# Kernel optimization log

Hardware: AMD Instinct MI355X
Metric: run time of the kernel (lower is better)

The kernel has to match this reference:

```python
import jax, jax.numpy as jnp
import numpy as np

NBINS = 256


def _getmask(mi):
    # mi: [h, w] image already scaled to [0, 255]
    # torch.histc(mi, bins=256, min=0, max=255): values outside [0,255] ignored
    hist = jax.lax.stop_gradient(
        jnp.histogram(mi, bins=NBINS, range=(0.0, 255.0))[0].astype(jnp.float32)
    )
    # mask_output[i] = sum_j |j - i| * hist[j]  -> small 256x256 matvec
    j = jnp.arange(NBINS, dtype=jnp.float32)
    dist = jnp.abs(j[:, None] - j[None, :])  # [256, 256]
    mask_output = dist @ hist                 # [256]
    # mask[image==i] = mask_output[i]; only exact-integer pixels in [0,255] match
    r = jnp.round(mi)
    valid = (mi == r) & (r >= 0.0) & (r <= 255.0)
    idx = jnp.clip(r, 0.0, 255.0).astype(jnp.int32)
    mask = jnp.where(valid, mask_output[idx], 0.0)
    # if mask.max()==0: return zeros; else return the (scaled) image itself
    return jnp.where(mask.max() == 0.0, jnp.zeros_like(mi), mi)


def _forward(image_irr, image_vis):
    irr = image_irr * 255.0
    _vis = image_vis * 255.0  # computed but unused in the original forward
    mi = irr[:, 0, :, :]                       # [b, h, w]
    masked = jax.vmap(_getmask)(mi) / 255.0    # [b, h, w]
    msk_ir = masked[:, None, :, :]             # [b, 1, h, w]
    msk = jnp.stack([msk_ir, 1.0 - msk_ir], axis=0)  # [2, b, 1, h, w]
    msks = jax.nn.softmax(msk, axis=0)
    return msks[0], msks[1]


def setup_inputs() -> dict:
    key = jax.random.key(0)
    k1, k2 = jax.random.split(key)
    shape = (16, 1, 1024, 1024)
    # quantized pixels so that image*255 is (mostly) exactly integer,
    # matching the module's implicit assumption (histc + equality tests)
    image_irr = jax.random.randint(k1, shape, 0, 256).astype(jnp.float32) / 255.0
    image_vis = jax.random.randint(k2, shape, 0, 256).astype(jnp.float32) / 255.0
    return {"image_irr": image_irr, "image_vis": image_vis}


def reference(image_irr, image_vis):
    return _forward(image_irr, image_vis)
```

## Files before the change

kernel.cpp:

```cpp
#include <hip/hip_runtime.h>
#include <stdint.h>

#define NBINS 256
#define BATCH 16
#define HW (1024*1024)
#define NPIX (BATCH * HW)
#define SCAN_BLOCKS 64

__global__ __launch_bounds__(256) void scan_kernel(const float* __restrict__ in,
                                                   uint2* __restrict__ partials) {
    __shared__ int smin[256], smax[256];
    __shared__ unsigned sval[256];
    const int tid = threadIdx.x;
    const int batch = blockIdx.y;

    int minb = 0x7FFF, maxb = -1;
    unsigned valid = 0;

    const float4* src = (const float4*)(in + (size_t)batch * HW) + (size_t)blockIdx.x * 4096;
    for (int i = tid; i < 4096; i += 256) {
        float4 x = src[i];
        float v[4] = {x.x, x.y, x.z, x.w};
#pragma unroll
        for (int k = 0; k < 4; ++k) {
            float mi = v[k] * 255.0f;
            if (mi >= 0.0f && mi <= 255.0f) {
                int b = (int)(mi * (256.0f / 255.0f));
                if (b > 255) b = 255;
                minb = min(minb, b);
                maxb = max(maxb, b);
                valid |= (mi == rintf(mi)) ? 1u : 0u;
            }
        }
    }
    smin[tid] = minb; smax[tid] = maxb; sval[tid] = valid;
    __syncthreads();
    for (int s = 128; s > 0; s >>= 1) {
        if (tid < s) {
            smin[tid] = min(smin[tid], smin[tid + s]);
            smax[tid] = max(smax[tid], smax[tid + s]);
            sval[tid] |= sval[tid + s];
        }
        __syncthreads();
    }
    if (tid == 0) {
        uint2 p;
        p.x = ((unsigned)(smin[0] & 0xFFFF) << 16) | (unsigned)(smax[0] & 0xFFFF);
        p.y = sval[0];
        partials[batch * SCAN_BLOCKS + blockIdx.x] = p;
    }
}

__global__ __launch_bounds__(64) void flag_kernel(const uint2* __restrict__ partials,
                                                  unsigned* __restrict__ flags) {
    const int b = blockIdx.x;
    const int t = threadIdx.x;
    uint2 p = partials[b * SCAN_BLOCKS + t];
    int minb = (int)(short)(p.x >> 16);
    int maxb = (int)(short)(p.x & 0xFFFF);
    unsigned valid = p.y;
#pragma unroll
    for (int off = 32; off > 0; off >>= 1) {
        minb = min(minb, __shfl_xor(minb, off));
        maxb = max(maxb, __shfl_xor(maxb, off));
        valid |= (unsigned)__shfl_xor((int)valid, off);
    }
    if (t == 0) flags[b] = (valid && (minb != maxb)) ? 1u : 0u;
}

__device__ __forceinline__ void softmax2(float x, unsigned flag, float& o0, float& o1) {
    float mi = x * 255.0f;
    float m = flag ? (mi / 255.0f) : 0.0f;
    float a = m;
    float b = 1.0f - m;
    float M = fmaxf(a, b);
    float e0 = expf(a - M);
    float e1 = expf(b - M);
    float s = e0 + e1;
    o0 = e0 / s;
    o1 = e1 / s;
}

__global__ __launch_bounds__(256) void out_kernel(const float* __restrict__ in,
                                                  const unsigned* __restrict__ flags,
                                                  float* __restrict__ out) {
    const size_t i4 = (size_t)blockIdx.x * 256 + threadIdx.x;
    const int batch = (int)(i4 >> 18);
    const unsigned f = flags[batch];
    float4 x = ((const float4*)in)[i4];
    float4 o0, o1;
    softmax2(x.x, f, o0.x, o1.x);
    softmax2(x.y, f, o0.y, o1.y);
    softmax2(x.z, f, o0.z, o1.z);
    softmax2(x.w, f, o0.w, o1.w);
    ((float4*)out)[i4] = o0;
    ((float4*)(out + (size_t)NPIX))[i4] = o1;
}

extern "C" void kernel_launch(void* const* d_in, const int* in_sizes, int n_in,
                              void* d_out, int out_size, void* d_ws, size_t ws_size,
                              hipStream_t stream) {
    const float* irr = (const float*)d_in[0];
    float* out = (float*)d_out;

    uint2* partials = (uint2*)d_ws;
    unsigned* flags = (unsigned*)(partials + BATCH * SCAN_BLOCKS);

    scan_kernel<<<dim3(SCAN_BLOCKS, BATCH), 256, 0, stream>>>(irr, partials);
    flag_kernel<<<BATCH, 64, 0, stream>>>(partials, flags);
    out_kernel<<<NPIX / 4 / 256, 256, 0, stream>>>(irr, flags, out);
}
```

Measured before the change: 230.5 us.

## Early-exit scan via global atomics once per-batch mask decision is known

The per-batch scan now accumulates min/max bin and validity into global atomics chunk by chunk. Every block stops reading as soon as the batch is known to have an exact-integer pixel and more than one occupied bin. This removes the separate flag kernel and most of the scan's reads on typical inputs, at the cost of a memset launch and atomic traffic. The output kernel also uses a simplified closed-form two-way softmax and nontemporal loads and stores.

```diff
diff --git a/kernel.cpp b/kernel.cpp
--- a/kernel.cpp
+++ b/kernel.cpp
@@ -1,25 +1,31 @@
 #include <hip/hip_runtime.h>
 #include <stdint.h>
 
-#define NBINS 256
 #define BATCH 16
 #define HW (1024*1024)
 #define NPIX (BATCH * HW)
-#define SCAN_BLOCKS 64
+#define SBLK 64
+
+typedef float vf4 __attribute__((ext_vector_type(4)));
+
+struct BState { unsigned valid, maxp1, maxc, done; };
 
 __global__ __launch_bounds__(256) void scan_kernel(const float* __restrict__ in,
-                                                   uint2* __restrict__ partials) {
-    __shared__ int smin[256], smax[256];
-    __shared__ unsigned sval[256];
+                                                   BState* __restrict__ st) {
     const int tid = threadIdx.x;
     const int batch = blockIdx.y;
+    BState* s = st + batch;
+    const vf4* src = (const vf4*)(in + (size_t)batch * HW) + (size_t)blockIdx.x * 4096;
+    __shared__ int sdone;
 
-    int minb = 0x7FFF, maxb = -1;
-    unsigned valid = 0;
+    for (int c = 0; c < 16; ++c) {
+        if (tid == 0)
+            sdone = (int)__hip_atomic_load(&s->done, __ATOMIC_RELAXED, __HIP_MEMORY_SCOPE_AGENT);
+        __syncthreads();
+        if (sdone) return;
 
-    const float4* src = (const float4*)(in + (size_t)batch * HW) + (size_t)blockIdx.x * 4096;
-    for (int i = tid; i < 4096; i += 256) {
-        float4 x = src[i];
+        vf4 x = src[c * 256 + tid];
+        int minb = 0x7FFF, maxb = -1, valid = 0;
         float v[4] = {x.x, x.y, x.z, x.w};
 #pragma unroll
         for (int k = 0; k < 4; ++k) {
@@ -29,72 +35,57 @@
                 if (b > 255) b = 255;
                 minb = min(minb, b);
                 maxb = max(maxb, b);
-                valid |= (mi == rintf(mi)) ? 1u : 0u;
+                valid |= (mi == rintf(mi)) ? 1 : 0;
             }
         }
-    }
-    smin[tid] = minb; smax[tid] = maxb; sval[tid] = valid;
-    __syncthreads();
-    for (int s = 128; s > 0; s >>= 1) {
-        if (tid < s) {
-            smin[tid] = min(smin[tid], smin[tid + s]);
-            smax[tid] = max(smax[tid], smax[tid + s]);
-            sval[tid] |= sval[tid + s];
+#pragma unroll
+        for (int off = 32; off > 0; off >>= 1) {
+            minb  = min(minb, __shfl_xor(minb, off));
+            maxb  = max(maxb, __shfl_xor(maxb, off));
+            valid |= __shfl_xor(valid, off);
+        }
+        if ((tid & 63) == 0) {
+            if (maxb >= 0) {
+                atomicMax(&s->maxp1, (unsigned)(maxb + 1));
+                atomicMax(&s->maxc,  (unsigned)(256 - minb));
+            }
+            if (valid) atomicOr(&s->valid, 1u);
         }
         __syncthreads();
-    }
-    if (tid == 0) {
-        uint2 p;
-        p.x = ((unsigned)(smin[0] & 0xFFFF) << 16) | (unsigned)(smax[0] & 0xFFFF);
-        p.y = sval[0];
-        partials[batch * SCAN_BLOCKS + blockIdx.x] = p;
+        if (tid == 0) {
+            unsigned v2 = __hip_atomic_load(&s->valid, __ATOMIC_RELAXED, __HIP_MEMORY_SCOPE_AGENT);
+            unsigned mp = __hip_atomic_load(&s->maxp1, __ATOMIC_RELAXED, __HIP_MEMORY_SCOPE_AGENT);
+            unsigned mc = __hip_atomic_load(&s->maxc,  __ATOMIC_RELAXED, __HIP_MEMORY_SCOPE_AGENT);
+            if (v2 && (mp + mc > 257))
+                __hip_atomic_store(&s->done, 1u, __ATOMIC_RELAXED, __HIP_MEMORY_SCOPE_AGENT);
+        }
     }
 }
 
-__global__ __launch_bounds__(64) void flag_kernel(const uint2* __restrict__ partials,
-                                                  unsigned* __restrict__ flags) {
-    const int b = blockIdx.x;
-    const int t = threadIdx.x;
-    uint2 p = partials[b * SCAN_BLOCKS + t];
-    int minb = (int)(short)(p.x >> 16);
-    int maxb = (int)(short)(p.x & 0xFFFF);
-    unsigned valid = p.y;
-#pragma unroll
-    for (int off = 32; off > 0; off >>= 1) {
-        minb = min(minb, __shfl_xor(minb, off));
-        maxb = max(maxb, __shfl_xor(maxb, off));
-        valid |= (unsigned)__shfl_xor((int)valid, off);
-    }
-    if (t == 0) flags[b] = (valid && (minb != maxb)) ? 1u : 0u;
-}
-
-__device__ __forceinline__ void softmax2(float x, unsigned flag, float& o0, float& o1) {
+__device__ __forceinline__ float2 softmax2(float x, float fm) {
     float mi = x * 255.0f;
-    float m = flag ? (mi / 255.0f) : 0.0f;
-    float a = m;
-    float b = 1.0f - m;
-    float M = fmaxf(a, b);
-    float e0 = expf(a - M);
-    float e1 = expf(b - M);
-    float s = e0 + e1;
-    o0 = e0 / s;
-    o1 = e1 / s;
+    float m = (mi / 255.0f) * fm;
+    float e = expf(1.0f - 2.0f * m);
+    float r = 1.0f / (1.0f + e);
+    return make_float2(r, e * r);
 }
 
 __global__ __launch_bounds__(256) void out_kernel(const float* __restrict__ in,
-                                                  const unsigned* __restrict__ flags,
+                                                  const BState* __restrict__ st,
                                                   float* __restrict__ out) {
+    const int batch = blockIdx.x >> 10;
+    const BState s = st[batch];
+    const float fm = (s.valid && (s.maxp1 + s.maxc > 257)) ? 1.0f : 0.0f;
     const size_t i4 = (size_t)blockIdx.x * 256 + threadIdx.x;
-    const int batch = (int)(i4 >> 18);
-    const unsigned f = flags[batch];
-    float4 x = ((const float4*)in)[i4];
-    float4 o0, o1;
-    softmax2(x.x, f, o0.x, o1.x);
-    softmax2(x.y, f, o0.y, o1.y);
-    softmax2(x.z, f, o0.z, o1.z);
-    softmax2(x.w, f, o0.w, o1.w);
-    ((float4*)out)[i4] = o0;
-    ((float4*)(out + (size_t)NPIX))[i4] = o1;
+    vf4 x = __builtin_nontemporal_load(&((const vf4*)in)[i4]);
+    float2 rx = softmax2(x.x, fm);
+    float2 ry = softmax2(x.y, fm);
+    float2 rz = softmax2(x.z, fm);
+    float2 rw = softmax2(x.w, fm);
+    vf4 o0 = {rx.x, ry.x, rz.x, rw.x};
+    vf4 o1 = {rx.y, ry.y, rz.y, rw.y};
+    __builtin_nontemporal_store(o0, &((vf4*)out)[i4]);
+    __builtin_nontemporal_store(o1, &((vf4*)(out + (size_t)NPIX))[i4]);
 }
 
 extern "C" void kernel_launch(void* const* d_in, const int* in_sizes, int n_in,
@@ -102,11 +93,9 @@
                               hipStream_t stream) {
     const float* irr = (const float*)d_in[0];
     float* out = (float*)d_out;
+    BState* st = (BState*)d_ws;
 
-    uint2* partials = (uint2*)d_ws;
-    unsigned* flags = (unsigned*)(partials + BATCH * SCAN_BLOCKS);
-
-    scan_kernel<<<dim3(SCAN_BLOCKS, BATCH), 256, 0, stream>>>(irr, partials);
-    flag_kernel<<<BATCH, 64, 0, stream>>>(partials, flags);
-    out_kernel<<<NPIX / 4 / 256, 256, 0, stream>>>(irr, flags, out);
+    (void)hipMemsetAsync(st, 0, BATCH * sizeof(BState), stream);
+    scan_kernel<<<dim3(SBLK, BATCH), 256, 0, stream>>>(irr, st);
+    out_kernel<<<NPIX / 4 / 256, 256, 0, stream>>>(irr, st, out);
 }
```

Result: slower. 383.4 us (+66.3%).
